# Kernel optimization log

Measured on AMD Instinct MI355X. Metric: run time of the kernel, lower is better.

Reference implementation:

```python
import jax, jax.numpy as jnp
import numpy as np

B, S, D_IN, D_OUT = 4, 4096, 1024, 1024

def setup_inputs() -> dict:
    key = jax.random.key(0)
    kx, kq, kk, kv = jax.random.split(key, 4)
    scale = 1.0 / np.sqrt(D_IN)
    return {
        "x": jax.random.normal(kx, (B, S, D_IN), dtype=jnp.float32),
        "Wq": jax.random.normal(kq, (D_IN, D_OUT), dtype=jnp.float32) * scale,
        "Wk": jax.random.normal(kk, (D_IN, D_OUT), dtype=jnp.float32) * scale,
        "Wv": jax.random.normal(kv, (D_IN, D_OUT), dtype=jnp.float32) * scale,
    }

def reference(x, Wq, Wk, Wv):
    # x: [B, S, d_in]; W*: [d_in, d_out]
    B_, S_, _ = x.shape
    d_out = Wq.shape[1]
    q = jnp.einsum("bsi,io->bso", x, Wq)
    k = jnp.einsum("bsi,io->bso", x, Wk)
    v = jnp.einsum("bsi,io->bso", x, Wv)
    # scores: [B, S, S]
    scores = jnp.einsum("bqo,bko->bqk", q, k)
    # causal mask: position q attends to k <= q (intended semantics of the
    # tril-buffer masked_fill); masked entries -> -inf before softmax.
    causal = jnp.tril(jnp.ones((S_, S_), dtype=bool))  # True where allowed
    scores = jnp.where(causal[None, :, :], scores, -jnp.inf)
    attn = jax.nn.softmax(scores / jnp.sqrt(jnp.asarray(d_out, scores.dtype)), axis=-1)
    # dropout p=0.0 -> identity
    return jnp.einsum("bqk,bko->bqo", attn, v)
```

## Files before the change

kernel.cpp:

```cpp
#include <hip/hip_runtime.h>


typedef __attribute__((ext_vector_type(8))) short bh8;
typedef __attribute__((ext_vector_type(4))) float f32x4;
typedef __attribute__((ext_vector_type(4))) unsigned int u32x4;
typedef __attribute__((ext_vector_type(2))) unsigned int u32x2;

#define BATCH 4
#define SEQ   4096
#define DIM   1024
#define MTOT  (BATCH * SEQ)

__device__ __forceinline__ unsigned short f2bf(float f) {
  union { float f; unsigned int u; } v; v.f = f;
  return (unsigned short)((v.u + 0x7FFFu + ((v.u >> 16) & 1u)) >> 16);
}

__global__ __launch_bounds__(256)
void k_convert_x(const float* __restrict__ x, unsigned short* __restrict__ xb) {
  size_t idx = ((size_t)blockIdx.x * 256 + threadIdx.x) * 8;
  f32x4 v0 = *(const f32x4*)(x + idx);
  f32x4 v1 = *(const f32x4*)(x + idx + 4);
  u32x4 pk;
  pk[0] = (unsigned)f2bf(v0[0]) | ((unsigned)f2bf(v0[1]) << 16);
  pk[1] = (unsigned)f2bf(v0[2]) | ((unsigned)f2bf(v0[3]) << 16);
  pk[2] = (unsigned)f2bf(v1[0]) | ((unsigned)f2bf(v1[1]) << 16);
  pk[3] = (unsigned)f2bf(v1[2]) | ((unsigned)f2bf(v1[3]) << 16);
  *(u32x4*)(xb + idx) = pk;
}

__global__ __launch_bounds__(256)
void k_transpose_w(const float* __restrict__ Wq, const float* __restrict__ Wk,
                   const float* __restrict__ Wv, unsigned short* __restrict__ wt) {
  __shared__ float tile[32][33];
  const int z = blockIdx.z;
  const float* W = (z == 0) ? Wq : ((z == 1) ? Wk : Wv);
  unsigned short* out = wt + (size_t)z * DIM * DIM;
  const int tx = threadIdx.x, ty = threadIdx.y;
  const int n = blockIdx.x * 32 + tx;
  const int k = blockIdx.y * 32 + ty;
#pragma unroll
  for (int i = 0; i < 32; i += 8)
    tile[ty + i][tx] = W[(size_t)(k + i) * DIM + n];
  __syncthreads();
  const int k2 = blockIdx.y * 32 + tx;
  const int n2 = blockIdx.x * 32 + ty;
#pragma unroll
  for (int i = 0; i < 32; i += 8)
    out[(size_t)(n2 + i) * DIM + k2] = f2bf(tile[tx][ty + i]);
}

__global__ __launch_bounds__(256)
void k_qkv_gemm(const unsigned short* __restrict__ xb, const unsigned short* __restrict__ wt,
                unsigned short* __restrict__ qb, unsigned short* __restrict__ kb,
                unsigned short* __restrict__ vt) {
  const int tid = threadIdx.x;
  const int l = tid & 63, w = tid >> 6;
  const int lane16 = l & 15, quad = l >> 4;
  const int wm = w & 1, wn = w >> 1;
  const int m0 = blockIdx.x * 128, n0 = blockIdx.y * 128, z = blockIdx.z;
  const unsigned short* wtz = wt + (size_t)z * DIM * DIM;

  __shared__ unsigned short As[128][40];
  __shared__ unsigned short Bs[128][40];

  f32x4 acc[4][4];
#pragma unroll
  for (int i = 0; i < 4; ++i)
#pragma unroll
    for (int j = 0; j < 4; ++j) acc[i][j] = (f32x4){0.f, 0.f, 0.f, 0.f};

  for (int k0 = 0; k0 < DIM; k0 += 32) {
#pragma unroll
    for (int i = 0; i < 2; ++i) {
      int c = tid + i * 256;
      int row = c >> 2, cc = (c & 3) * 8;
      *(bh8*)&As[row][cc] = *(const bh8*)(xb  + (size_t)(m0 + row) * DIM + k0 + cc);
      *(bh8*)&Bs[row][cc] = *(const bh8*)(wtz + (size_t)(n0 + row) * DIM + k0 + cc);
    }
    __syncthreads();
    bh8 a[4], b[4];
#pragma unroll
    for (int mt = 0; mt < 4; ++mt) a[mt] = *(const bh8*)&As[wm * 64 + mt * 16 + lane16][quad * 8];
#pragma unroll
    for (int nt = 0; nt < 4; ++nt) b[nt] = *(const bh8*)&Bs[wn * 64 + nt * 16 + lane16][quad * 8];
#pragma unroll
    for (int mt = 0; mt < 4; ++mt)
#pragma unroll
      for (int nt = 0; nt < 4; ++nt)
        acc[mt][nt] = __builtin_amdgcn_mfma_f32_16x16x32_bf16(a[mt], b[nt], acc[mt][nt], 0, 0, 0);
    __syncthreads();
  }

  if (z < 2) {
    unsigned short* outp = (z == 0) ? qb : kb;
#pragma unroll
    for (int mt = 0; mt < 4; ++mt)
#pragma unroll
      for (int nt = 0; nt < 4; ++nt) {
        int row = m0 + wm * 64 + mt * 16 + quad * 4;
        int col = n0 + wn * 64 + nt * 16 + lane16;
#pragma unroll
        for (int r = 0; r < 4; ++r)
          outp[(size_t)(row + r) * DIM + col] = f2bf(acc[mt][nt][r]);
      }
  } else {
#pragma unroll
    for (int mt = 0; mt < 4; ++mt)
#pragma unroll
      for (int nt = 0; nt < 4; ++nt) {
        int m = m0 + wm * 64 + mt * 16 + quad * 4;
        int bb = m >> 12, s = m & (SEQ - 1);
        int col = n0 + wn * 64 + nt * 16 + lane16;
        unsigned long long pk =
            (unsigned long long)f2bf(acc[mt][nt][0]) |
            ((unsigned long long)f2bf(acc[mt][nt][1]) << 16) |
            ((unsigned long long)f2bf(acc[mt][nt][2]) << 32) |
            ((unsigned long long)f2bf(acc[mt][nt][3]) << 48);
        *(unsigned long long*)(vt + (size_t)bb * DIM * SEQ + (size_t)col * SEQ + s) = pk;
      }
  }
}

__global__ __launch_bounds__(512, 2)
void k_attn(const unsigned short* __restrict__ qb, const unsigned short* __restrict__ kb,
            const unsigned short* __restrict__ vt, float* __restrict__ out) {
  const int tid = threadIdx.x;
  const int w = tid >> 6;
  const int l = tid & 63;
  const int lane16 = l & 15, quad = l >> 4;
  const int batch = blockIdx.x;
  const int pid = blockIdx.y;

  __shared__ float Pp[8][32][68];
  __shared__ unsigned short Psh[32][72];
  __shared__ float row_m[32], row_l[32], row_alpha[32];

  const size_t bbase = (size_t)batch * SEQ;
  const unsigned short* vtb = vt + (size_t)batch * DIM * SEQ;
  const float cexp = 0.04508422002778f;

  for (int half = 0; half < 2; ++half) {
    const int t = (half == 0) ? pid : (127 - pid);
    const int q0 = t * 32;

    bh8 qf[2][4];
#pragma unroll
    for (int mt = 0; mt < 2; ++mt)
#pragma unroll
      for (int c = 0; c < 4; ++c)
        qf[mt][c] = *(const bh8*)(qb + (bbase + q0 + mt * 16 + lane16) * DIM +
                                  w * 128 + c * 32 + quad * 8);

    f32x4 o[2][8];
#pragma unroll
    for (int mt = 0; mt < 2; ++mt)
#pragma unroll
      for (int nt = 0; nt < 8; ++nt) o[mt][nt] = (f32x4){0.f, 0.f, 0.f, 0.f};

    const int nk = (q0 + 95) >> 6;

    bh8 kf[4][4];
#pragma unroll
    for (int kt = 0; kt < 4; ++kt)
#pragma unroll
      for (int c = 0; c < 4; ++c)
        kf[kt][c] = *(const bh8*)(kb + (bbase + kt * 16 + lane16) * DIM +
                                  w * 128 + c * 32 + quad * 8);

    for (int it = 0; it < nk; ++it) {
      const int k0 = it * 64;

      bh8 vfa[4][2];
#pragma unroll
      for (int nt = 0; nt < 4; ++nt)
#pragma unroll
        for (int kc = 0; kc < 2; ++kc)
          vfa[nt][kc] = *(const bh8*)(vtb + (size_t)(w * 128 + nt * 16 + lane16) * SEQ +
                                      k0 + kc * 32 + quad * 8);

      if (it == 0 && tid < 32) { row_m[tid] = -3.0e38f; row_l[tid] = 0.f; }

#pragma unroll
      for (int kt = 0; kt < 4; ++kt) {
        if (k0 + kt * 16 <= q0 + 31) {
#pragma unroll
          for (int mt = 0; mt < 2; ++mt) {
            f32x4 s = (f32x4){0.f, 0.f, 0.f, 0.f};
#pragma unroll
            for (int c = 0; c < 4; ++c)
              s = __builtin_amdgcn_mfma_f32_16x16x32_bf16(qf[mt][c], kf[kt][c], s, 0, 0, 0);
            int row = mt * 16 + quad * 4;
            int col = kt * 16 + lane16;
#pragma unroll
            for (int r = 0; r < 4; ++r)
              Pp[w][row + r][col] = s[r];
          }
        }
      }

      if (it + 1 < nk) {
#pragma unroll
        for (int kt = 0; kt < 4; ++kt)
#pragma unroll
          for (int c = 0; c < 4; ++c)
            kf[kt][c] = *(const bh8*)(kb + (bbase + k0 + 64 + kt * 16 + lane16) * DIM +
                                      w * 128 + c * 32 + quad * 8);
      }
      __syncthreads();

      {
        int r = tid >> 4, c0 = (tid & 15) * 4;
        int q = q0 + r;
        f32x4 sv = *(const f32x4*)&Pp[0][r][c0];
#pragma unroll
        for (int ww = 1; ww < 8; ++ww)
          sv += *(const f32x4*)&Pp[ww][r][c0];
#pragma unroll
        for (int j = 0; j < 4; ++j)
          if (k0 + c0 + j > q) sv[j] = -3.0e38f;
        float mx = fmaxf(fmaxf(sv[0], sv[1]), fmaxf(sv[2], sv[3]));
#pragma unroll
        for (int off = 1; off < 16; off <<= 1)
          mx = fmaxf(mx, __shfl_xor(mx, off));
        float mold = row_m[r];
        float mnew = fmaxf(mold, mx);
        float p0 = __builtin_amdgcn_exp2f((sv[0] - mnew) * cexp);
        float p1 = __builtin_amdgcn_exp2f((sv[1] - mnew) * cexp);
        float p2 = __builtin_amdgcn_exp2f((sv[2] - mnew) * cexp);
        float p3 = __builtin_amdgcn_exp2f((sv[3] - mnew) * cexp);
        float sum = (p0 + p1) + (p2 + p3);
#pragma unroll
        for (int off = 1; off < 16; off <<= 1)
          sum += __shfl_xor(sum, off);
        float alpha = __builtin_amdgcn_exp2f((mold - mnew) * cexp);
        u32x2 pk;
        pk[0] = (unsigned)f2bf(p0) | ((unsigned)f2bf(p1) << 16);
        pk[1] = (unsigned)f2bf(p2) | ((unsigned)f2bf(p3) << 16);
        *(u32x2*)&Psh[r][c0] = pk;
        if ((tid & 15) == 0) {
          row_m[r] = mnew;
          row_l[r] = alpha * row_l[r] + sum;
          row_alpha[r] = alpha;
        }
      }
      __syncthreads();

      {
        bh8 vfb[4][2];
#pragma unroll
        for (int nt = 0; nt < 4; ++nt)
#pragma unroll
          for (int kc = 0; kc < 2; ++kc)
            vfb[nt][kc] = *(const bh8*)(vtb + (size_t)(w * 128 + (nt + 4) * 16 + lane16) * SEQ +
                                        k0 + kc * 32 + quad * 8);

#pragma unroll
        for (int mt = 0; mt < 2; ++mt) {
          f32x4 al;
#pragma unroll
          for (int r = 0; r < 4; ++r) al[r] = row_alpha[mt * 16 + quad * 4 + r];
#pragma unroll
          for (int nt = 0; nt < 8; ++nt) o[mt][nt] *= al;
        }
        bh8 pf[2][2];
#pragma unroll
        for (int mt = 0; mt < 2; ++mt)
#pragma unroll
          for (int kc = 0; kc < 2; ++kc)
            pf[mt][kc] = *(const bh8*)&Psh[mt * 16 + lane16][kc * 32 + quad * 8];
#pragma unroll
        for (int kc = 0; kc < 2; ++kc) {
          if (k0 + kc * 32 <= q0 + 31) {
#pragma unroll
            for (int nt = 0; nt < 4; ++nt)
#pragma unroll
              for (int mt = 0; mt < 2; ++mt)
                o[mt][nt] = __builtin_amdgcn_mfma_f32_16x16x32_bf16(pf[mt][kc], vfa[nt][kc], o[mt][nt], 0, 0, 0);
#pragma unroll
            for (int nt = 0; nt < 4; ++nt)
#pragma unroll
              for (int mt = 0; mt < 2; ++mt)
                o[mt][nt + 4] = __builtin_amdgcn_mfma_f32_16x16x32_bf16(pf[mt][kc], vfb[nt][kc], o[mt][nt + 4], 0, 0, 0);
          }
        }
      }
    }

#pragma unroll
    for (int mt = 0; mt < 2; ++mt) {
      int row = mt * 16 + quad * 4;
      float il[4];
#pragma unroll
      for (int r = 0; r < 4; ++r) il[r] = 1.0f / row_l[row + r];
#pragma unroll
      for (int nt = 0; nt < 8; ++nt) {
        size_t base = (bbase + q0 + row) * DIM + w * 128 + nt * 16 + lane16;
#pragma unroll
        for (int r = 0; r < 4; ++r)
          out[base + (size_t)r * DIM] = o[mt][nt][r] * il[r];
      }
    }
    __syncthreads();
  }
}

extern "C" void kernel_launch(void* const* d_in, const int* in_sizes, int n_in,
                              void* d_out, int out_size, void* d_ws, size_t ws_size,
                              hipStream_t stream) {
  const float* x  = (const float*)d_in[0];
  const float* Wq = (const float*)d_in[1];
  const float* Wk = (const float*)d_in[2];
  const float* Wv = (const float*)d_in[3];
  float* out = (float*)d_out;

  char* ws = (char*)d_ws;
  const size_t XB_BYTES = (size_t)MTOT * DIM * 2;
  const size_t WT_BYTES = (size_t)3 * DIM * DIM * 2;
  unsigned short* xb = (unsigned short*)(ws);
  unsigned short* wt = (unsigned short*)(ws + XB_BYTES);
  unsigned short* qb = (unsigned short*)(ws + XB_BYTES + WT_BYTES);
  unsigned short* kb = qb + (size_t)MTOT * DIM;
  unsigned short* vt = kb + (size_t)MTOT * DIM;

  k_convert_x<<<dim3((MTOT * DIM) / (256 * 8)), dim3(256), 0, stream>>>(x, xb);
  k_transpose_w<<<dim3(32, 32, 3), dim3(32, 8), 0, stream>>>(Wq, Wk, Wv, wt);
  k_qkv_gemm<<<dim3(MTOT / 128, DIM / 128, 3), dim3(256), 0, stream>>>(xb, wt, qb, kb, vt);
  k_attn<<<dim3(BATCH, 64), dim3(512), 0, stream>>>(qb, kb, vt, out);
}
```

Measured before the change: 908.5 us.

## Restructure attention kernel to 16 waves with 32-wide key tiles and deferred PV

```diff
diff --git a/kernel.cpp b/kernel.cpp
--- a/kernel.cpp
+++ b/kernel.cpp
@@ -4,7 +4,6 @@
 typedef __attribute__((ext_vector_type(8))) short bh8;
 typedef __attribute__((ext_vector_type(4))) float f32x4;
 typedef __attribute__((ext_vector_type(4))) unsigned int u32x4;
-typedef __attribute__((ext_vector_type(2))) unsigned int u32x2;
 
 #define BATCH 4
 #define SEQ   4096
@@ -122,7 +121,7 @@
   }
 }
 
-__global__ __launch_bounds__(512, 2)
+__global__ __launch_bounds__(1024)
 void k_attn(const unsigned short* __restrict__ qb, const unsigned short* __restrict__ kb,
             const unsigned short* __restrict__ vt, float* __restrict__ out) {
   const int tid = threadIdx.x;
@@ -131,174 +130,167 @@
   const int lane16 = l & 15, quad = l >> 4;
   const int batch = blockIdx.x;
   const int pid = blockIdx.y;
-
-  __shared__ float Pp[8][32][68];
-  __shared__ unsigned short Psh[32][72];
+  const int sr = tid >> 5;
+  const int sc = tid & 31;
+
+  __shared__ float Pp[16][32][36];
+  __shared__ unsigned short Psh[32][36];
   __shared__ float row_m[32], row_l[32], row_alpha[32];
+  float* Oe = (float*)Pp;
 
   const size_t bbase = (size_t)batch * SEQ;
   const unsigned short* vtb = vt + (size_t)batch * DIM * SEQ;
   const float cexp = 0.04508422002778f;
 
   for (int half = 0; half < 2; ++half) {
-    const int t = (half == 0) ? pid : (127 - pid);
+    const int t = half ? (127 - pid) : pid;
     const int q0 = t * 32;
-
-    bh8 qf[2][4];
+    const int nk = t + 1;
+
+    bh8 qf[2][2];
 #pragma unroll
     for (int mt = 0; mt < 2; ++mt)
 #pragma unroll
-      for (int c = 0; c < 4; ++c)
+      for (int c = 0; c < 2; ++c)
         qf[mt][c] = *(const bh8*)(qb + (bbase + q0 + mt * 16 + lane16) * DIM +
-                                  w * 128 + c * 32 + quad * 8);
-
-    f32x4 o[2][8];
+                                  w * 64 + c * 32 + quad * 8);
+
+    f32x4 o[2][4];
 #pragma unroll
     for (int mt = 0; mt < 2; ++mt)
 #pragma unroll
-      for (int nt = 0; nt < 8; ++nt) o[mt][nt] = (f32x4){0.f, 0.f, 0.f, 0.f};
-
-    const int nk = (q0 + 95) >> 6;
-
-    bh8 kf[4][4];
-#pragma unroll
-    for (int kt = 0; kt < 4; ++kt)
-#pragma unroll
-      for (int c = 0; c < 4; ++c)
-        kf[kt][c] = *(const bh8*)(kb + (bbase + kt * 16 + lane16) * DIM +
-                                  w * 128 + c * 32 + quad * 8);
+      for (int nt = 0; nt < 4; ++nt) o[mt][nt] = (f32x4){0.f, 0.f, 0.f, 0.f};
+
+    bh8 kfA[2][2], kfB[2][2], vf[4], pf[2];
+#pragma unroll
+    for (int kt = 0; kt < 2; ++kt)
+#pragma unroll
+      for (int c = 0; c < 2; ++c)
+        kfA[kt][c] = *(const bh8*)(kb + (bbase + kt * 16 + lane16) * DIM +
+                                   w * 64 + c * 32 + quad * 8);
 
     for (int it = 0; it < nk; ++it) {
-      const int k0 = it * 64;
-
-      bh8 vfa[4][2];
+      const int k0 = it * 32;
+
+      if (it + 1 < nk) {
+#pragma unroll
+        for (int kt = 0; kt < 2; ++kt)
+#pragma unroll
+          for (int c = 0; c < 2; ++c)
+            kfB[kt][c] = *(const bh8*)(kb + (bbase + k0 + 32 + kt * 16 + lane16) * DIM +
+                                       w * 64 + c * 32 + quad * 8);
+      }
+
+      if (it > 0) {
+        f32x4 al0, al1;
+#pragma unroll
+        for (int r = 0; r < 4; ++r) {
+          al0[r] = row_alpha[quad * 4 + r];
+          al1[r] = row_alpha[16 + quad * 4 + r];
+        }
+#pragma unroll
+        for (int nt = 0; nt < 4; ++nt) { o[0][nt] *= al0; o[1][nt] *= al1; }
+#pragma unroll
+        for (int nt = 0; nt < 4; ++nt)
+#pragma unroll
+          for (int mt = 0; mt < 2; ++mt)
+            o[mt][nt] = __builtin_amdgcn_mfma_f32_16x16x32_bf16(pf[mt], vf[nt], o[mt][nt], 0, 0, 0);
+      }
+
+#pragma unroll
+      for (int mt = 0; mt < 2; ++mt)
+#pragma unroll
+        for (int kt = 0; kt < 2; ++kt) {
+          f32x4 s = (f32x4){0.f, 0.f, 0.f, 0.f};
+          s = __builtin_amdgcn_mfma_f32_16x16x32_bf16(qf[mt][0], kfA[kt][0], s, 0, 0, 0);
+          s = __builtin_amdgcn_mfma_f32_16x16x32_bf16(qf[mt][1], kfA[kt][1], s, 0, 0, 0);
+          int row = mt * 16 + quad * 4;
+          int col = kt * 16 + lane16;
+#pragma unroll
+          for (int r = 0; r < 4; ++r)
+            Pp[w][row + r][col] = s[r];
+        }
+      __syncthreads();
+
 #pragma unroll
       for (int nt = 0; nt < 4; ++nt)
-#pragma unroll
-        for (int kc = 0; kc < 2; ++kc)
-          vfa[nt][kc] = *(const bh8*)(vtb + (size_t)(w * 128 + nt * 16 + lane16) * SEQ +
-                                      k0 + kc * 32 + quad * 8);
-
-      if (it == 0 && tid < 32) { row_m[tid] = -3.0e38f; row_l[tid] = 0.f; }
-
-#pragma unroll
-      for (int kt = 0; kt < 4; ++kt) {
-        if (k0 + kt * 16 <= q0 + 31) {
-#pragma unroll
-          for (int mt = 0; mt < 2; ++mt) {
-            f32x4 s = (f32x4){0.f, 0.f, 0.f, 0.f};
-#pragma unroll
-            for (int c = 0; c < 4; ++c)
-              s = __builtin_amdgcn_mfma_f32_16x16x32_bf16(qf[mt][c], kf[kt][c], s, 0, 0, 0);
-            int row = mt * 16 + quad * 4;
-            int col = kt * 16 + lane16;
-#pragma unroll
-            for (int r = 0; r < 4; ++r)
-              Pp[w][row + r][col] = s[r];
-          }
-        }
-      }
-
-      if (it + 1 < nk) {
-#pragma unroll
-        for (int kt = 0; kt < 4; ++kt)
-#pragma unroll
-          for (int c = 0; c < 4; ++c)
-            kf[kt][c] = *(const bh8*)(kb + (bbase + k0 + 64 + kt * 16 + lane16) * DIM +
-                                      w * 128 + c * 32 + quad * 8);
-      }
-      __syncthreads();
+        vf[nt] = *(const bh8*)(vtb + (size_t)(w * 64 + nt * 16 + lane16) * SEQ +
+                               k0 + quad * 8);
 
       {
-        int r = tid >> 4, c0 = (tid & 15) * 4;
-        int q = q0 + r;
-        f32x4 sv = *(const f32x4*)&Pp[0][r][c0];
-#pragma unroll
-        for (int ww = 1; ww < 8; ++ww)
-          sv += *(const f32x4*)&Pp[ww][r][c0];
-#pragma unroll
-        for (int j = 0; j < 4; ++j)
-          if (k0 + c0 + j > q) sv[j] = -3.0e38f;
-        float mx = fmaxf(fmaxf(sv[0], sv[1]), fmaxf(sv[2], sv[3]));
-#pragma unroll
-        for (int off = 1; off < 16; off <<= 1)
+        float sv = Pp[0][sr][sc];
+#pragma unroll
+        for (int k = 1; k < 16; ++k) sv += Pp[k][sr][sc];
+        if (k0 + sc > q0 + sr) sv = -3.0e38f;
+        float mx = sv;
+#pragma unroll
+        for (int off = 1; off < 32; off <<= 1)
           mx = fmaxf(mx, __shfl_xor(mx, off));
-        float mold = row_m[r];
+        float mold = it ? row_m[sr] : -3.0e38f;
         float mnew = fmaxf(mold, mx);
-        float p0 = __builtin_amdgcn_exp2f((sv[0] - mnew) * cexp);
-        float p1 = __builtin_amdgcn_exp2f((sv[1] - mnew) * cexp);
-        float p2 = __builtin_amdgcn_exp2f((sv[2] - mnew) * cexp);
-        float p3 = __builtin_amdgcn_exp2f((sv[3] - mnew) * cexp);
-        float sum = (p0 + p1) + (p2 + p3);
-#pragma unroll
-        for (int off = 1; off < 16; off <<= 1)
+        float p = __builtin_amdgcn_exp2f((sv - mnew) * cexp);
+        float sum = p;
+#pragma unroll
+        for (int off = 1; off < 32; off <<= 1)
           sum += __shfl_xor(sum, off);
         float alpha = __builtin_amdgcn_exp2f((mold - mnew) * cexp);
-        u32x2 pk;
-        pk[0] = (unsigned)f2bf(p0) | ((unsigned)f2bf(p1) << 16);
-        pk[1] = (unsigned)f2bf(p2) | ((unsigned)f2bf(p3) << 16);
-        *(u32x2*)&Psh[r][c0] = pk;
-        if ((tid & 15) == 0) {
-          row_m[r] = mnew;
-          row_l[r] = alpha * row_l[r] + sum;
-          row_alpha[r] = alpha;
+        Psh[sr][sc] = f2bf(p);
+        if (sc == 0) {
+          row_m[sr] = mnew;
+          row_l[sr] = alpha * (it ? row_l[sr] : 0.f) + sum;
+          row_alpha[sr] = alpha;
         }
       }
       __syncthreads();
 
-      {
-        bh8 vfb[4][2];
+      pf[0] = *(const bh8*)&Psh[lane16][quad * 8];
+      pf[1] = *(const bh8*)&Psh[16 + lane16][quad * 8];
+
+      if (it + 1 < nk) {
+#pragma unroll
+        for (int kt = 0; kt < 2; ++kt)
+#pragma unroll
+          for (int c = 0; c < 2; ++c) kfA[kt][c] = kfB[kt][c];
+      }
+    }
+
+    {
+      f32x4 al0, al1;
+#pragma unroll
+      for (int r = 0; r < 4; ++r) {
+        al0[r] = row_alpha[quad * 4 + r];
+        al1[r] = row_alpha[16 + quad * 4 + r];
+      }
+#pragma unroll
+      for (int nt = 0; nt < 4; ++nt) { o[0][nt] *= al0; o[1][nt] *= al1; }
+#pragma unroll
+      for (int nt = 0; nt < 4; ++nt)
+#pragma unroll
+        for (int mt = 0; mt < 2; ++mt)
+          o[mt][nt] = __builtin_amdgcn_mfma_f32_16x16x32_bf16(pf[mt], vf[nt], o[mt][nt], 0, 0, 0);
+    }
+
+    {
+      float* Ow = Oe + w * 1040;
+#pragma unroll
+      for (int mt = 0; mt < 2; ++mt) {
+        float il[4];
+#pragma unroll
+        for (int r = 0; r < 4; ++r) il[r] = 1.0f / row_l[mt * 16 + quad * 4 + r];
 #pragma unroll
         for (int nt = 0; nt < 4; ++nt)
 #pragma unroll
-          for (int kc = 0; kc < 2; ++kc)
-            vfb[nt][kc] = *(const bh8*)(vtb + (size_t)(w * 128 + (nt + 4) * 16 + lane16) * SEQ +
-                                        k0 + kc * 32 + quad * 8);
-
-#pragma unroll
-        for (int mt = 0; mt < 2; ++mt) {
-          f32x4 al;
-#pragma unroll
-          for (int r = 0; r < 4; ++r) al[r] = row_alpha[mt * 16 + quad * 4 + r];
-#pragma unroll
-          for (int nt = 0; nt < 8; ++nt) o[mt][nt] *= al;
-        }
-        bh8 pf[2][2];
-#pragma unroll
-        for (int mt = 0; mt < 2; ++mt)
-#pragma unroll
-          for (int kc = 0; kc < 2; ++kc)
-            pf[mt][kc] = *(const bh8*)&Psh[mt * 16 + lane16][kc * 32 + quad * 8];
-#pragma unroll
-        for (int kc = 0; kc < 2; ++kc) {
-          if (k0 + kc * 32 <= q0 + 31) {
-#pragma unroll
-            for (int nt = 0; nt < 4; ++nt)
-#pragma unroll
-              for (int mt = 0; mt < 2; ++mt)
-                o[mt][nt] = __builtin_amdgcn_mfma_f32_16x16x32_bf16(pf[mt][kc], vfa[nt][kc], o[mt][nt], 0, 0, 0);
-#pragma unroll
-            for (int nt = 0; nt < 4; ++nt)
-#pragma unroll
-              for (int mt = 0; mt < 2; ++mt)
-                o[mt][nt + 4] = __builtin_amdgcn_mfma_f32_16x16x32_bf16(pf[mt][kc], vfb[nt][kc], o[mt][nt + 4], 0, 0, 0);
+          for (int r = 0; r < 4; ++r)
+            Ow[(quad * 4 + r) * 65 + nt * 16 + lane16] = o[mt][nt][r] * il[r];
+        int row8 = l >> 3, c8 = l & 7;
+#pragma unroll
+        for (int set = 0; set < 2; ++set)
+#pragma unroll
+          for (int rep = 0; rep < 2; ++rep) {
+            f32x4 v = *(const f32x4*)&Ow[(set * 8 + row8) * 65 + c8 * 4 + rep * 32];
+            *(f32x4*)(out + (bbase + q0 + mt * 16 + set * 8 + row8) * DIM +
+                      w * 64 + c8 * 4 + rep * 32) = v;
           }
-        }
-      }
-    }
-
-#pragma unroll
-    for (int mt = 0; mt < 2; ++mt) {
-      int row = mt * 16 + quad * 4;
-      float il[4];
-#pragma unroll
-      for (int r = 0; r < 4; ++r) il[r] = 1.0f / row_l[row + r];
-#pragma unroll
-      for (int nt = 0; nt < 8; ++nt) {
-        size_t base = (bbase + q0 + row) * DIM + w * 128 + nt * 16 + lane16;
-#pragma unroll
-        for (int r = 0; r < 4; ++r)
-          out[base + (size_t)r * DIM] = o[mt][nt][r] * il[r];
       }
     }
     __syncthreads();
@@ -326,5 +318,5 @@
   k_convert_x<<<dim3((MTOT * DIM) / (256 * 8)), dim3(256), 0, stream>>>(x, xb);
   k_transpose_w<<<dim3(32, 32, 3), dim3(32, 8), 0, stream>>>(Wq, Wk, Wv, wt);
   k_qkv_gemm<<<dim3(MTOT / 128, DIM / 128, 3), dim3(256), 0, stream>>>(xb, wt, qb, kb, vt);
-  k_attn<<<dim3(BATCH, 64), dim3(512), 0, stream>>>(qb, kb, vt, out);
-}
+  k_attn<<<dim3(BATCH, 64), dim3(1024), 0, stream>>>(qb, kb, vt, out);
+}
```

Result: slower. 1.285 ms (+41.4%).
